# Kernel tuning notes

Measured on AMD Instinct MI355X. Metric: run time of the kernel, lower is better.

The kernel has to match this reference:

```python
import jax, jax.numpy as jnp
import numpy as np

R = 4          # args.search_range
D = 2 * R + 1  # window size per axis -> D*D = 81 output channels


def setup_inputs() -> dict:
    key = jax.random.key(0)
    k1, k2 = jax.random.split(key)
    B, C, H, W = 4, 128, 64, 128
    src = jax.random.normal(k1, (B, C, H, W), dtype=jnp.float32)
    tgt = jax.random.normal(k2, (B, C, H, W), dtype=jnp.float32)
    return {"src": src, "tgt": tgt}


def reference(src, tgt):
    # Faithful to the torch code: tgt is zero-padded by R on each spatial side,
    # then for output pixel (i, j) the window indices into the PADDED tensor are
    # I in [i-R, i+R], J in [j-R, j+R]. For i < R the index is negative, which in
    # torch wraps around -> reproduce with modular indexing.
    B, C, H, W = src.shape
    tp = jnp.pad(tgt, ((0, 0), (0, 0), (R, R), (R, R)))  # [B,C,H+2R,W+2R]
    Hp, Wp = H + 2 * R, W + 2 * R
    # col_idx[dj, j] = (j - R + dj) mod Wp
    col_idx = (jnp.arange(W)[None, :] - R + jnp.arange(D)[:, None]) % Wp  # [D,W]
    outs = []
    for di in range(D):  # small fixed loop over 9 row offsets
        row_idx = (jnp.arange(H) - R + di) % Hp        # [H]
        t_rows = tp[:, :, row_idx, :]                  # [B,C,H,Wp]
        t_win = t_rows[:, :, :, col_idx]               # [B,C,H,D,W]
        # channel-dot-product per pixel and per column offset
        outs.append(jnp.einsum('bchdw,bchw->bdhw', t_win, src))
    # channel ordering k = di*D + dj matches the original double loop over (I, J)
    return jnp.concatenate(outs, axis=1)  # [B, D*D, H, W]
```

## Files before the change

### kernel.cpp

```cpp
#include <hip/hip_runtime.h>
#include <stdint.h>

#define NB 4
#define NC 128
#define NH 64
#define NW 128
#define ND 9
#define NOUT (ND * ND)

#define TH 8
#define TW 16
#define CCH 8
#define NCHUNK (NC / CCH)
#define TGT_F4 768
#define SRC_F4 256
#define SRC_OFF 3072
#define BUF_F 4096

__global__ __launch_bounds__(320, 1)
void costvol_kernel(const float* __restrict__ src,
                    const float* __restrict__ tgt,
                    float* __restrict__ out) {
  __shared__ float lds[2][BUF_F];

  const int tid = threadIdx.x;
  const int bid = blockIdx.x;
  const int b  = bid >> 6;
  const int tile = bid & 63;
  const int h0 = (tile >> 3) * TH;
  const int w0 = (tile & 7) * TW;

  const int di = tid >> 5;
  const int q  = tid & 31;
  const int r  = q >> 2;
  const int qc = q & 3;

  float acc[ND][4];
#pragma unroll
  for (int dj = 0; dj < ND; ++dj)
#pragma unroll
    for (int k = 0; k < 4; ++k) acc[dj][k] = 0.0f;

  float4 treg[3];
  float4 sreg;

  auto load_regs = [&](int chunk) {
    const int c0 = chunk * CCH;
#pragma unroll
    for (int j = 0; j < 3; ++j) {
      const int i = tid + j * 320;
      if (i < TGT_F4) {
        const int ch = i / 96;
        const int rem = i - ch * 96;
        const int row = rem / 6;
        const int cq = rem - row * 6;
        const int y = h0 - 8 + row;
        const int x = w0 - 8 + 4 * cq;
        if (y >= 0 && x >= 0) {
          treg[j] = *(const float4*)(tgt + (size_t)(((b * NC + c0 + ch) * NH + y) * NW + x));
        } else {
          treg[j] = make_float4(0.f, 0.f, 0.f, 0.f);
        }
      }
    }
    if (tid < SRC_F4) {
      const int ch = tid >> 5;
      const int rem = tid & 31;
      const int row = rem >> 2;
      const int cq = rem & 3;
      sreg = *(const float4*)(src + (size_t)(((b * NC + c0 + ch) * NH + h0 + row) * NW + w0 + 4 * cq));
    }
  };

  auto write_lds = [&](int buf) {
#pragma unroll
    for (int j = 0; j < 3; ++j) {
      const int i = tid + j * 320;
      if (i < TGT_F4) *(float4*)&lds[buf][4 * i] = treg[j];
    }
    if (tid < SRC_F4) *(float4*)&lds[buf][SRC_OFF + 4 * tid] = sreg;
  };

  load_regs(0);
  write_lds(0);
  int cur = 0;

  for (int k = 0; k < NCHUNK; ++k) {
    if (k + 1 < NCHUNK) load_regs(k + 1);
    __syncthreads();

    if (di < ND) {
      const float* sb = &lds[cur][SRC_OFF + r * TW + 4 * qc];
      const float* tb = &lds[cur][(r + di) * 24 + 4 * qc];
#pragma unroll
      for (int ch = 0; ch < CCH; ++ch) {
        const float4 sv = *(const float4*)(sb + ch * (TH * TW));
        const float* tp = tb + ch * 384;
        const float4 t0 = *(const float4*)(tp);
        const float4 t1 = *(const float4*)(tp + 4);
        const float4 t2 = *(const float4*)(tp + 8);
        float t[12];
        t[0] = t0.x; t[1] = t0.y; t[2]  = t0.z; t[3]  = t0.w;
        t[4] = t1.x; t[5] = t1.y; t[6]  = t1.z; t[7]  = t1.w;
        t[8] = t2.x; t[9] = t2.y; t[10] = t2.z; t[11] = t2.w;
#pragma unroll
        for (int dj = 0; dj < ND; ++dj) {
          acc[dj][0] = fmaf(sv.x, t[dj + 0], acc[dj][0]);
          acc[dj][1] = fmaf(sv.y, t[dj + 1], acc[dj][1]);
          acc[dj][2] = fmaf(sv.z, t[dj + 2], acc[dj][2]);
          acc[dj][3] = fmaf(sv.w, t[dj + 3], acc[dj][3]);
        }
      }
    }

    if (k + 1 < NCHUNK) write_lds(cur ^ 1);
    cur ^= 1;
  }

  if (di < ND) {
#pragma unroll
    for (int dj = 0; dj < ND; ++dj) {
      float4 o;
      o.x = acc[dj][0]; o.y = acc[dj][1]; o.z = acc[dj][2]; o.w = acc[dj][3];
      *(float4*)(out + (size_t)(((b * NOUT + di * ND + dj) * NH + h0 + r) * NW + w0 + 4 * qc)) = o;
    }
  }
}

extern "C" void kernel_launch(void* const* d_in, const int* in_sizes, int n_in,
                              void* d_out, int out_size, void* d_ws, size_t ws_size,
                              hipStream_t stream) {
  const float* src = (const float*)d_in[0];
  const float* tgt = (const float*)d_in[1];
  float* out = (float*)d_out;
  costvol_kernel<<<dim3(NB * (NH / TH) * (NW / TW)), dim3(320), 0, stream>>>(src, tgt, out);
}
```

Measured before the change: 105.2 us.

## Retile cost volume by full-width rows, channel split with atomics and DPP shifts

Each block now covers four full-width output rows for one quarter of the channels, so 256 blocks of 576 threads replace the 8x16 spatial tiles. Each thread computes 8 adjacent pixels and gets the left-neighbour window values from the previous lane through a DPP row shift, instead of loading overlapping halos from LDS. Partial sums from the four channel groups are combined with global float atomics into an output that is first cleared with a memset. This is meant to cut redundant halo loads and raise per-thread reuse, at the cost of extra atomic traffic on a large output and an additional memset pass.

```diff
diff --git a/kernel.cpp b/kernel.cpp
--- a/kernel.cpp
+++ b/kernel.cpp
@@ -6,79 +6,112 @@
 #define NH 64
 #define NW 128
 #define ND 9
-#define NOUT (ND * ND)
+#define NOUT 81
 
-#define TH 8
-#define TW 16
-#define CCH 8
-#define NCHUNK (NC / CCH)
-#define TGT_F4 768
-#define SRC_F4 256
-#define SRC_OFF 3072
-#define BUF_F 4096
+#define NHB 4
+#define CQ 32
+#define CCH 4
+#define NCHUNK (CQ / CCH)
+#define TROWS (NHB + 8)
+#define LSTR 132
+#define TGT_FL (CCH * TROWS * LSTR)
+#define SRC_FL (CCH * NHB * LSTR)
+#define SRC_OFF TGT_FL
+#define BUF_FL (TGT_FL + SRC_FL)
+#define TGT_F4 (CCH * TROWS * 32)
+#define ALL_F4 (TGT_F4 + CCH * NHB * 32)
 
-__global__ __launch_bounds__(320, 1)
+__device__ __forceinline__ float prev_lane(float x) {
+  int yi = __builtin_amdgcn_update_dpp(0, __float_as_int(x), 0x111, 0xf, 0xf, true);
+  return __int_as_float(yi);
+}
+
+__device__ __forceinline__ void atomic_fadd(float* p, float v) {
+#if defined(__has_builtin) && __has_builtin(__builtin_amdgcn_global_atomic_fadd_f32)
+  __builtin_amdgcn_global_atomic_fadd_f32(p, v);
+#else
+  atomicAdd(p, v);
+#endif
+}
+
+__global__ __launch_bounds__(576, 1)
 void costvol_kernel(const float* __restrict__ src,
                     const float* __restrict__ tgt,
                     float* __restrict__ out) {
-  __shared__ float lds[2][BUF_F];
+  __shared__ float lds[2][BUF_FL];
 
   const int tid = threadIdx.x;
   const int bid = blockIdx.x;
-  const int b  = bid >> 6;
-  const int tile = bid & 63;
-  const int h0 = (tile >> 3) * TH;
-  const int w0 = (tile & 7) * TW;
+  const int hg = bid >> 4;
+  const int bc = bid & 15;
+  const int b  = bc >> 2;
+  const int cq = bc & 3;
+  const int h0 = hg * NHB;
+  const int c0 = cq * CQ;
 
-  const int di = tid >> 5;
-  const int q  = tid & 31;
-  const int r  = q >> 2;
-  const int qc = q & 3;
+  const int di = tid >> 6;
+  const int r  = (tid >> 4) & 3;
+  const int ql = tid & 15;
 
-  float acc[ND][4];
+  float acc[ND][8];
 #pragma unroll
   for (int dj = 0; dj < ND; ++dj)
 #pragma unroll
-    for (int k = 0; k < 4; ++k) acc[dj][k] = 0.0f;
+    for (int p = 0; p < 8; ++p) acc[dj][p] = 0.0f;
 
-  float4 treg[3];
-  float4 sreg;
+  float4 sreg[4];
 
   auto load_regs = [&](int chunk) {
-    const int c0 = chunk * CCH;
+    const int cb = c0 + chunk * CCH;
 #pragma unroll
-    for (int j = 0; j < 3; ++j) {
-      const int i = tid + j * 320;
-      if (i < TGT_F4) {
-        const int ch = i / 96;
-        const int rem = i - ch * 96;
-        const int row = rem / 6;
-        const int cq = rem - row * 6;
-        const int y = h0 - 8 + row;
-        const int x = w0 - 8 + 4 * cq;
-        if (y >= 0 && x >= 0) {
-          treg[j] = *(const float4*)(tgt + (size_t)(((b * NC + c0 + ch) * NH + y) * NW + x));
+    for (int p = 0; p < 4; ++p) {
+      const int j = tid + p * 576;
+      if (j < ALL_F4) {
+        float4 v = make_float4(0.f, 0.f, 0.f, 0.f);
+        if (j < TGT_F4) {
+          const int ch = j / 384;
+          const int rem = j - ch * 384;
+          const int row = rem >> 5;
+          const int q = rem & 31;
+          const int y = h0 - 8 + row;
+          if (y >= 0)
+            v = *(const float4*)(tgt + (size_t)(((b * NC + cb + ch) * NH + y) * NW + 4 * q));
         } else {
-          treg[j] = make_float4(0.f, 0.f, 0.f, 0.f);
+          const int k2 = j - TGT_F4;
+          const int ch = k2 >> 7;
+          const int rem = k2 & 127;
+          const int row = rem >> 5;
+          const int q = rem & 31;
+          v = *(const float4*)(src + (size_t)(((b * NC + cb + ch) * NH + h0 + row) * NW + 4 * q));
         }
+        sreg[p] = v;
       }
-    }
-    if (tid < SRC_F4) {
-      const int ch = tid >> 5;
-      const int rem = tid & 31;
-      const int row = rem >> 2;
-      const int cq = rem & 3;
-      sreg = *(const float4*)(src + (size_t)(((b * NC + c0 + ch) * NH + h0 + row) * NW + w0 + 4 * cq));
     }
   };
 
   auto write_lds = [&](int buf) {
 #pragma unroll
-    for (int j = 0; j < 3; ++j) {
-      const int i = tid + j * 320;
-      if (i < TGT_F4) *(float4*)&lds[buf][4 * i] = treg[j];
+    for (int p = 0; p < 4; ++p) {
+      const int j = tid + p * 576;
+      if (j < ALL_F4) {
+        float* dst;
+        if (j < TGT_F4) {
+          const int ch = j / 384;
+          const int rem = j - ch * 384;
+          const int row = rem >> 5;
+          const int q = rem & 31;
+          dst = &lds[buf][(ch * TROWS + row) * LSTR + 4 * q];
+        } else {
+          const int k2 = j - TGT_F4;
+          const int ch = k2 >> 7;
+          const int rem = k2 & 127;
+          const int row = rem >> 5;
+          const int q = rem & 31;
+          dst = &lds[buf][SRC_OFF + (ch * NHB + row) * LSTR + 4 * q];
+        }
+        *(float4*)dst = sreg[p];
+      }
     }
-    if (tid < SRC_F4) *(float4*)&lds[buf][SRC_OFF + 4 * tid] = sreg;
   };
 
   load_regs(0);
@@ -86,30 +119,29 @@
   int cur = 0;
 
   for (int k = 0; k < NCHUNK; ++k) {
+    __syncthreads();
     if (k + 1 < NCHUNK) load_regs(k + 1);
-    __syncthreads();
 
-    if (di < ND) {
-      const float* sb = &lds[cur][SRC_OFF + r * TW + 4 * qc];
-      const float* tb = &lds[cur][(r + di) * 24 + 4 * qc];
+    {
+      const float* Lt = &lds[cur][(r + di) * LSTR + 8 * ql];
+      const float* Ls = &lds[cur][SRC_OFF + r * LSTR + 8 * ql];
 #pragma unroll
       for (int ch = 0; ch < CCH; ++ch) {
-        const float4 sv = *(const float4*)(sb + ch * (TH * TW));
-        const float* tp = tb + ch * 384;
-        const float4 t0 = *(const float4*)(tp);
-        const float4 t1 = *(const float4*)(tp + 4);
-        const float4 t2 = *(const float4*)(tp + 8);
-        float t[12];
-        t[0] = t0.x; t[1] = t0.y; t[2]  = t0.z; t[3]  = t0.w;
-        t[4] = t1.x; t[5] = t1.y; t[6]  = t1.z; t[7]  = t1.w;
-        t[8] = t2.x; t[9] = t2.y; t[10] = t2.z; t[11] = t2.w;
+        const float4 ta = *(const float4*)(Lt + ch * (TROWS * LSTR));
+        const float4 tb = *(const float4*)(Lt + ch * (TROWS * LSTR) + 4);
+        const float4 sa = *(const float4*)(Ls + ch * (NHB * LSTR));
+        const float4 sb = *(const float4*)(Ls + ch * (NHB * LSTR) + 4);
+        float w16[16];
+        w16[8]  = ta.x; w16[9]  = ta.y; w16[10] = ta.z; w16[11] = ta.w;
+        w16[12] = tb.x; w16[13] = tb.y; w16[14] = tb.z; w16[15] = tb.w;
 #pragma unroll
-        for (int dj = 0; dj < ND; ++dj) {
-          acc[dj][0] = fmaf(sv.x, t[dj + 0], acc[dj][0]);
-          acc[dj][1] = fmaf(sv.y, t[dj + 1], acc[dj][1]);
-          acc[dj][2] = fmaf(sv.z, t[dj + 2], acc[dj][2]);
-          acc[dj][3] = fmaf(sv.w, t[dj + 3], acc[dj][3]);
-        }
+        for (int i = 0; i < 8; ++i) w16[i] = prev_lane(w16[8 + i]);
+        float s[8] = {sa.x, sa.y, sa.z, sa.w, sb.x, sb.y, sb.z, sb.w};
+#pragma unroll
+        for (int dj = 0; dj < ND; ++dj)
+#pragma unroll
+          for (int p = 0; p < 8; ++p)
+            acc[dj][p] = fmaf(s[p], w16[p + dj], acc[dj][p]);
       }
     }
 
@@ -117,12 +149,12 @@
     cur ^= 1;
   }
 
-  if (di < ND) {
+  if (h0 + r + di >= 8) {
 #pragma unroll
     for (int dj = 0; dj < ND; ++dj) {
-      float4 o;
-      o.x = acc[dj][0]; o.y = acc[dj][1]; o.z = acc[dj][2]; o.w = acc[dj][3];
-      *(float4*)(out + (size_t)(((b * NOUT + di * ND + dj) * NH + h0 + r) * NW + w0 + 4 * qc)) = o;
+      float* op = out + (size_t)(((b * NOUT + di * ND + dj) * NH + h0 + r) * NW + 8 * ql);
+#pragma unroll
+      for (int p = 0; p < 8; ++p) atomic_fadd(op + p, acc[dj][p]);
     }
   }
 }
@@ -133,5 +165,6 @@
   const float* src = (const float*)d_in[0];
   const float* tgt = (const float*)d_in[1];
   float* out = (float*)d_out;
-  costvol_kernel<<<dim3(NB * (NH / TH) * (NW / TW)), dim3(320), 0, stream>>>(src, tgt, out);
+  hipMemsetAsync(d_out, 0, (size_t)out_size * sizeof(float), stream);
+  costvol_kernel<<<dim3(256), dim3(576), 0, stream>>>(src, tgt, out);
 }
```

After: 379.4 us. 261% more time.
